# Performance work log

Measured on AMD Instinct MI355X. Metric: run time of the kernel, lower is better.

The kernel has to match this reference:

```python
import jax, jax.numpy as jnp
import numpy as np

WS = 7        # window size (square)
SH = 3        # shift size
NH = 8        # num heads
N = WS * WS   # tokens per window


def _rel_pos_index():
    coords = np.stack(np.meshgrid(np.arange(WS), np.arange(WS), indexing='ij'))
    cf = coords.reshape(2, -1)                      # (2, N)
    rel = cf[:, :, None] - cf[:, None, :]           # (2, N, N)
    rel = rel.transpose(1, 2, 0)
    rel[:, :, 0] += WS - 1
    rel[:, :, 1] += WS - 1
    rel[:, :, 0] *= 2 * WS - 1
    return rel.sum(-1)                              # (N, N) int


def _attn_mask(pH, pW):
    img = np.zeros((pH, pW), dtype=np.float32)
    h_sl = [(0, pH - WS), (pH - WS, pH - SH), (pH - SH, pH)]
    w_sl = [(0, pW - WS), (pW - WS, pW - SH), (pW - SH, pW)]
    cnt = 0
    for h0, h1 in h_sl:
        for w0, w1 in w_sl:
            img[h0:h1, w0:w1] = cnt
            cnt += 1
    m = img.reshape(pH // WS, WS, pW // WS, WS).transpose(0, 2, 1, 3).reshape(-1, N)
    diff = m[:, None, :] - m[:, :, None]            # (nw, N, N)
    return np.where(diff != 0, -100.0, 0.0).astype(np.float32)


def setup_inputs() -> dict:
    key = jax.random.key(0)
    ks = jax.random.split(key, 6)
    C = 256
    return {
        'x': jax.random.normal(ks[0], (32, 56, 56, C), dtype=jnp.float32),
        'qkv_weight': jax.random.normal(ks[1], (3 * C, C), dtype=jnp.float32) * 0.02,
        'qkv_bias': jax.random.normal(ks[2], (3 * C,), dtype=jnp.float32) * 0.02,
        'proj_weight': jax.random.normal(ks[3], (C, C), dtype=jnp.float32) * 0.02,
        'proj_bias': jax.random.normal(ks[4], (C,), dtype=jnp.float32) * 0.02,
        'rpb_table': jax.random.normal(ks[5], ((2 * WS - 1) ** 2, NH), dtype=jnp.float32) * 0.02,
    }


def reference(x, qkv_weight, qkv_bias, proj_weight, proj_bias, rpb_table):
    B, H, W, C = x.shape
    hd = C // NH
    pad_r = (WS - W % WS) % WS
    pad_b = (WS - H % WS) % WS
    xp = jnp.pad(x, ((0, 0), (0, pad_b), (0, pad_r), (0, 0)))
    pH, pW = H + pad_b, W + pad_r
    xp = jnp.roll(xp, shift=(-SH, -SH), axis=(1, 2))
    nw = (pH // WS) * (pW // WS)
    # window partition -> (B*nw, N, C)
    xw = xp.reshape(B, pH // WS, WS, pW // WS, WS, C)
    xw = xw.transpose(0, 1, 3, 2, 4, 5).reshape(B * nw, N, C)
    # qkv projection
    qkv = xw @ qkv_weight.T + qkv_bias                      # (B*nw, N, 3C)
    qkv = qkv.reshape(B * nw, N, 3, NH, hd).transpose(2, 0, 3, 1, 4)
    q, k, v = qkv[0], qkv[1], qkv[2]                        # (B*nw, NH, N, hd)
    q = q * (hd ** -0.5)
    attn = jnp.einsum('bhnd,bhmd->bhnm', q, k)              # (B*nw, NH, N, N)
    # relative position bias
    idx = jnp.asarray(_rel_pos_index())
    bias = rpb_table[idx].transpose(2, 0, 1)                # (NH, N, N)
    attn = attn + bias[None]
    # shift mask
    mask = jnp.asarray(_attn_mask(pH, pW))                  # (nw, N, N)
    attn = attn.reshape(B, nw, NH, N, N) + mask[None, :, None]
    attn = jax.nn.softmax(attn.reshape(B * nw, NH, N, N), axis=-1)
    out = jnp.einsum('bhnm,bhmd->bhnd', attn, v)            # (B*nw, NH, N, hd)
    out = out.transpose(0, 2, 1, 3).reshape(B * nw, N, C)
    out = out @ proj_weight.T + proj_bias
    # window reverse
    out = out.reshape(B, pH // WS, pW // WS, WS, WS, C)
    out = out.transpose(0, 1, 3, 2, 4, 5).reshape(B, pH, pW, C)
    out = jnp.roll(out, shift=(SH, SH), axis=(1, 2))
    return out[:, :H, :W, :]
```

## Files before the change

kernel.cpp:

```cpp
#include <hip/hip_runtime.h>
#include <hip/hip_bf16.h>

typedef __attribute__((ext_vector_type(4))) float f32x4;
typedef __attribute__((ext_vector_type(8))) short s16x8;
typedef __attribute__((ext_vector_type(4))) short s16x4;
typedef __attribute__((ext_vector_type(4))) unsigned uintx4;

#define LBS 264
#define VTS 72
#define LOS 132

__device__ __forceinline__ unsigned cvt2bf(float a, float b) {
    unsigned r;
    asm("v_cvt_pk_bf16_f32 %0, %1, %2" : "=v"(r) : "v"(a), "v"(b));
    return r;
}

__device__ __forceinline__ s16x4 pk4bf(float a, float b, float c, float d) {
    uint2 t = { cvt2bf(a, b), cvt2bf(c, d) };
    return __builtin_bit_cast(s16x4, t);
}

__device__ __forceinline__ s16x8 expand_z(s16x4 c) {
    uint2 u = __builtin_bit_cast(uint2, c);
    uintx4 r = { u.x & 0xFFFFu, u.x >> 16, u.y & 0xFFFFu, u.y >> 16 };
    return __builtin_bit_cast(s16x8, r);
}

__global__ void prep_kernel(const float* __restrict__ qw, const float* __restrict__ pw,
                            const float* __restrict__ rpb,
                            short* __restrict__ wqkv, short* __restrict__ wproj,
                            float* __restrict__ bm) {
    int idx = blockIdx.x * blockDim.x + threadIdx.x;
    if (idx < 65536) {
        const float* src = (idx < 49152) ? (qw + idx * 4) : (pw + (idx - 49152) * 4);
        unsigned* dst = (unsigned*)((idx < 49152) ? (wqkv + idx * 4) : (wproj + (idx - 49152) * 4));
        const f32x4 v = *(const f32x4*)src;
        uint2 o = { cvt2bf(v.x, v.y), cvt2bf(v.z, v.w) };
        *(uint2*)dst = o;
    } else {
        int k = idx - 65536;
        int j = k & 63;
        int i = (k >> 6) & 63;
        int h = (k >> 12) & 7;
        int c = k >> 15;
        int cy = c >> 1, cx = c & 1;
        float v;
        if (j >= 49) {
            v = -1e9f;
        } else {
            int ic = i > 48 ? 48 : i;
            int yi = ic / 7, xi = ic % 7;
            int yj = j / 7, xj = j % 7;
            float bias = rpb[((yi - yj + 6) * 13 + (xi - xj + 6)) * 8 + h];
            int ri = (cy ? (yi < 4 ? 1 : 2) : 0) * 3 + (cx ? (xi < 4 ? 1 : 2) : 0);
            int rj = (cy ? (yj < 4 ? 1 : 2) : 0) * 3 + (cx ? (xj < 4 ? 1 : 2) : 0);
            float mask = (ri != rj) ? -100.0f : 0.0f;
            v = (bias + mask) * 1.4426950408889634f;
        }
        bm[k] = v;
    }
}

__global__ __launch_bounds__(512, 2)
void attn_kernel(const float* __restrict__ x,
                 const float* __restrict__ qkv_bias,
                 const short* __restrict__ wqkv,
                 const float* __restrict__ bm,
                 unsigned short* __restrict__ la) {
    __shared__ __align__(16) short buf[64 * LBS];
    __shared__ __align__(16) short lvt[128 * VTS];
    __shared__ float lml[8 * 64];

    const int tid  = threadIdx.x;
    const int w    = tid >> 6;
    const int lane = tid & 63;
    const int il   = lane & 15;
    const int gl   = lane >> 4;
    const int hl   = w >> 1;
    const int jh   = w & 1;

    const int hg  = blockIdx.x & 1;
    const int win = blockIdx.x >> 1;
    const int wid = win & 63;
    const int b   = win >> 6;
    const int wy  = wid >> 3, wx = wid & 7;

    for (int i = tid; i < 4096; i += 512) {
        int t = i >> 6, c4 = (i & 63) << 2;
        uint2 o;
        if (t < 49) {
            int ty = t / 7, tx = t % 7;
            int R = wy * 7 + ty + 3; if (R >= 56) R -= 56;
            int C = wx * 7 + tx + 3; if (C >= 56) C -= 56;
            const f32x4 v = *(const f32x4*)(x + (((b * 56 + R) * 56 + C) << 8) + c4);
            o.x = cvt2bf(v.x, v.y); o.y = cvt2bf(v.z, v.w);
        } else {
            o.x = 0; o.y = 0;
        }
        *(uint2*)&buf[t * LBS + c4] = o;
    }
    __syncthreads();

    {
        f32x4 acc[4][3];
        #pragma unroll
        for (int mi = 0; mi < 4; mi++)
            #pragma unroll
            for (int t = 0; t < 3; t++) acc[mi][t] = (f32x4){0.f, 0.f, 0.f, 0.f};
        __builtin_amdgcn_s_setprio(1);
        for (int k0 = 0; k0 < 256; k0 += 32) {
            s16x8 a[4];
            #pragma unroll
            for (int mi = 0; mi < 4; mi++)
                a[mi] = *(const s16x8*)&buf[(mi * 16 + il) * LBS + k0 + 8 * gl];
            #pragma unroll
            for (int t = 0; t < 3; t++) {
                s16x8 bfr = *(const s16x8*)(wqkv + (t * 256 + hg * 128 + 16 * w + il) * 256 + k0 + 8 * gl);
                #pragma unroll
                for (int mi = 0; mi < 4; mi++)
                    acc[mi][t] = __builtin_amdgcn_mfma_f32_16x16x32_bf16(a[mi], bfr, acc[mi][t], 0, 0, 0);
            }
        }
        __builtin_amdgcn_s_setprio(0);
        {
            float bv = qkv_bias[512 + hg * 128 + 16 * w + il];
            #pragma unroll
            for (int mi = 0; mi < 4; mi++)
                *(s16x4*)&lvt[(16 * w + il) * VTS + mi * 16 + gl * 4] =
                    pk4bf(acc[mi][2][0] + bv, acc[mi][2][1] + bv,
                          acc[mi][2][2] + bv, acc[mi][2][3] + bv);
        }
        __syncthreads();
        {
            const float QSCL = 0.17677669529663687f * 1.4426950408889634f;
            float bq_ = qkv_bias[hg * 128 + 16 * w + il];
            float bk_ = qkv_bias[256 + hg * 128 + 16 * w + il];
            #pragma unroll
            for (int mi = 0; mi < 4; mi++)
                #pragma unroll
                for (int r = 0; r < 4; r++) {
                    int row = mi * 16 + gl * 4 + r;
                    unsigned u = cvt2bf((acc[mi][0][r] + bq_) * QSCL, acc[mi][1][r] + bk_);
                    buf[row * LBS + 16 * w + il] = (short)u;
                    buf[row * LBS + 128 + 16 * w + il] = (short)(u >> 16);
                }
        }
    }
    __syncthreads();

    const int cls = ((wy == 7) ? 2 : 0) + ((wx == 7) ? 1 : 0);
    const float* bmp = bm + ((cls * 8 + hg * 4 + hl) * 64) * 64;

    f32x4 s[2][4];
    #pragma unroll
    for (int mi = 0; mi < 2; mi++)
        #pragma unroll
        for (int ni = 0; ni < 4; ni++)
            s[mi][ni] = *(const f32x4*)&bmp[(ni * 16 + il) * 64 + jh * 32 + mi * 16 + gl * 4];
    {
        s16x8 bq[4];
        #pragma unroll
        for (int ni = 0; ni < 4; ni++)
            bq[ni] = *(const s16x8*)&buf[(ni * 16 + il) * LBS + hl * 32 + 8 * gl];
        __builtin_amdgcn_s_setprio(1);
        #pragma unroll
        for (int mi = 0; mi < 2; mi++) {
            s16x8 ak = *(const s16x8*)&buf[(jh * 32 + mi * 16 + il) * LBS + 128 + hl * 32 + 8 * gl];
            #pragma unroll
            for (int ni = 0; ni < 4; ni++)
                s[mi][ni] = __builtin_amdgcn_mfma_f32_16x16x32_bf16(ak, bq[ni], s[mi][ni], 0, 0, 0);
        }
        __builtin_amdgcn_s_setprio(0);
    }
    float l[4] = { 0.f, 0.f, 0.f, 0.f };
    s16x4 pkd[2][4];
    #pragma unroll
    for (int mi = 0; mi < 2; mi++)
        #pragma unroll
        for (int ni = 0; ni < 4; ni++) {
            float p0 = exp2f(s[mi][ni][0]);
            float p1 = exp2f(s[mi][ni][1]);
            float p2 = exp2f(s[mi][ni][2]);
            float p3 = exp2f(s[mi][ni][3]);
            l[ni] += (p0 + p1) + (p2 + p3);
            pkd[mi][ni] = pk4bf(p0, p1, p2, p3);
        }
    #pragma unroll
    for (int ni = 0; ni < 4; ni++) {
        l[ni] += __shfl_xor(l[ni], 16);
        l[ni] += __shfl_xor(l[ni], 32);
    }
    if (jh == 0 && gl == 0) {
        #pragma unroll
        for (int ni = 0; ni < 4; ni++) lml[(hl * 2) * 64 + ni * 16 + il] = l[ni];
    }
    __syncthreads();

    f32x4 o[2][4];
    #pragma unroll
    for (int md = 0; md < 2; md++)
        #pragma unroll
        for (int ni = 0; ni < 4; ni++) o[md][ni] = (f32x4){0.f, 0.f, 0.f, 0.f};
    __builtin_amdgcn_s_setprio(1);
    #pragma unroll
    for (int mi = 0; mi < 2; mi++) {
        s16x8 av[2];
        #pragma unroll
        for (int md = 0; md < 2; md++)
            av[md] = expand_z(*(const s16x4*)&lvt[(hl * 32 + md * 16 + il) * VTS + jh * 32 + mi * 16 + 4 * gl]);
        #pragma unroll
        for (int ni = 0; ni < 4; ni++) {
            s16x8 bp = expand_z(pkd[mi][ni]);
            #pragma unroll
            for (int md = 0; md < 2; md++)
                o[md][ni] = __builtin_amdgcn_mfma_f32_16x16x32_bf16(av[md], bp, o[md][ni], 0, 0, 0);
        }
    }
    __builtin_amdgcn_s_setprio(0);
    float* lout = (float*)buf;
    if (jh == 0) {
        #pragma unroll
        for (int md = 0; md < 2; md++)
            #pragma unroll
            for (int ni = 0; ni < 4; ni++)
                *(f32x4*)&lout[(ni * 16 + il) * LOS + hl * 32 + md * 16 + gl * 4] = o[md][ni];
    }
    __syncthreads();
    if (jh == 1) {
        float sc[4];
        #pragma unroll
        for (int ni = 0; ni < 4; ni++)
            sc[ni] = __builtin_amdgcn_rcpf(l[ni] + lml[(hl * 2) * 64 + ni * 16 + il]);
        #pragma unroll
        for (int ni = 0; ni < 4; ni++) {
            int i = ni * 16 + il;
            if (i < 49) {
                #pragma unroll
                for (int md = 0; md < 2; md++) {
                    f32x4 t = *(const f32x4*)&lout[i * LOS + hl * 32 + md * 16 + gl * 4];
                    uint2 pk = { cvt2bf((t.x + o[md][ni][0]) * sc[ni], (t.y + o[md][ni][1]) * sc[ni]),
                                 cvt2bf((t.z + o[md][ni][2]) * sc[ni], (t.w + o[md][ni][3]) * sc[ni]) };
                    *(uint2*)&la[(win * 49 + i) * 256 + hg * 128 + hl * 32 + md * 16 + gl * 4] = pk;
                }
            }
        }
    }
}

__global__ __launch_bounds__(512, 2)
void proj_kernel(const unsigned short* __restrict__ la,
                 const float* __restrict__ proj_bias,
                 const short* __restrict__ wproj,
                 float* __restrict__ out) {
    __shared__ __align__(16) short buf[64 * LBS];

    const int tid  = threadIdx.x;
    const int w    = tid >> 6;
    const int lane = tid & 63;
    const int il   = lane & 15;
    const int gl   = lane >> 4;

    const int win = blockIdx.x;
    const int wid = win & 63;
    const int b   = win >> 6;
    const int wy  = wid >> 3, wx = wid & 7;

    for (int i = tid; i < 2048; i += 512) {
        int t = i >> 5, c8 = (i & 31) << 3;
        uintx4 v = (t < 49) ? *(const uintx4*)&la[(win * 49 + t) * 256 + c8]
                            : (uintx4){0u, 0u, 0u, 0u};
        *(uintx4*)&buf[t * LBS + c8] = v;
    }
    __syncthreads();

    f32x4 acc[4][2];
    #pragma unroll
    for (int mi = 0; mi < 4; mi++)
        #pragma unroll
        for (int ni = 0; ni < 2; ni++) acc[mi][ni] = (f32x4){0.f, 0.f, 0.f, 0.f};
    __builtin_amdgcn_s_setprio(1);
    for (int k0 = 0; k0 < 256; k0 += 32) {
        s16x8 a[4];
        #pragma unroll
        for (int mi = 0; mi < 4; mi++)
            a[mi] = *(const s16x8*)&buf[(mi * 16 + il) * LBS + k0 + 8 * gl];
        #pragma unroll
        for (int ni = 0; ni < 2; ni++) {
            s16x8 bw = *(const s16x8*)(wproj + (32 * w + 16 * ni + il) * 256 + k0 + 8 * gl);
            #pragma unroll
            for (int mi = 0; mi < 4; mi++)
                acc[mi][ni] = __builtin_amdgcn_mfma_f32_16x16x32_bf16(a[mi], bw, acc[mi][ni], 0, 0, 0);
        }
    }
    __builtin_amdgcn_s_setprio(0);
    __syncthreads();
    #pragma unroll
    for (int ni = 0; ni < 2; ni++) {
        int oc = 32 * w + 16 * ni + il;
        float pb = proj_bias[oc];
        #pragma unroll
        for (int mi = 0; mi < 4; mi++)
            #pragma unroll
            for (int r = 0; r < 4; r++) {
                int t = mi * 16 + gl * 4 + r;
                if (t < 49) {
                    unsigned u = cvt2bf(acc[mi][ni][r] + pb, 0.f);
                    buf[t * LBS + oc] = (short)u;
                }
            }
    }
    __syncthreads();
    for (int i = tid; i < 1568; i += 512) {
        int t = i >> 5, c8 = (i & 31) << 3;
        uintx4 u = *(const uintx4*)&buf[t * LBS + c8];
        f32x4 v0, v1;
        v0.x = __builtin_bit_cast(float, u.x << 16);
        v0.y = __builtin_bit_cast(float, u.x & 0xFFFF0000u);
        v0.z = __builtin_bit_cast(float, u.y << 16);
        v0.w = __builtin_bit_cast(float, u.y & 0xFFFF0000u);
        v1.x = __builtin_bit_cast(float, u.z << 16);
        v1.y = __builtin_bit_cast(float, u.z & 0xFFFF0000u);
        v1.z = __builtin_bit_cast(float, u.w << 16);
        v1.w = __builtin_bit_cast(float, u.w & 0xFFFF0000u);
        int ty = t / 7, tx = t % 7;
        int R = wy * 7 + ty + 3; if (R >= 56) R -= 56;
        int C = wx * 7 + tx + 3; if (C >= 56) C -= 56;
        float* op = out + (((b * 56 + R) * 56 + C) << 8) + c8;
        *(f32x4*)op = v0;
        *(f32x4*)(op + 4) = v1;
    }
}

extern "C" void kernel_launch(void* const* d_in, const int* in_sizes, int n_in,
                              void* d_out, int out_size, void* d_ws, size_t ws_size,
                              hipStream_t stream) {
    const float* x   = (const float*)d_in[0];
    const float* qw  = (const float*)d_in[1];
    const float* qb  = (const float*)d_in[2];
    const float* pw  = (const float*)d_in[3];
    const float* pb  = (const float*)d_in[4];
    const float* rpb = (const float*)d_in[5];

    short* wqkv  = (short*)d_ws;
    short* wproj = wqkv + 768 * 256;
    float* bmt   = (float*)((char*)d_ws + 524288);
    unsigned short* lat = (unsigned short*)((char*)d_ws + 2097152);

    prep_kernel<<<768, 256, 0, stream>>>(qw, pw, rpb, wqkv, wproj, bmt);
    attn_kernel<<<4096, 512, 0, stream>>>(x, qb, wqkv, bmt, lat);
    proj_kernel<<<2048, 512, 0, stream>>>(lat, pb, wproj, (float*)d_out);
}
```

Measured before the change: 234.8 us.

## Split QKV projection into a row-contiguous kernel writing windowed bf16 Q/K/V

Moves the QKV GEMM out of the attention kernel into a new kernel that processes one contiguous image row (56 tokens) per block, so the fp32 input is read with coalesced row accesses instead of shifted window gathers. It then scatters bf16 Q/K and V into per-window, per-head-group buffers that the attention kernel loads and transposes into LDS, and the attention output reuses the Q/K buffer. Also drops the s_setprio hints. This adds an extra kernel launch and a bf16 round trip of Q/K/V through global memory.

```diff
diff --git a/kernel.cpp b/kernel.cpp
--- a/kernel.cpp
+++ b/kernel.cpp
@@ -7,6 +7,7 @@
 typedef __attribute__((ext_vector_type(4))) unsigned uintx4;
 
 #define LBS 264
+#define VBS 136
 #define VTS 72
 #define LOS 132
 
@@ -63,42 +64,42 @@
 }
 
 __global__ __launch_bounds__(512, 2)
-void attn_kernel(const float* __restrict__ x,
-                 const float* __restrict__ qkv_bias,
-                 const short* __restrict__ wqkv,
-                 const float* __restrict__ bm,
-                 unsigned short* __restrict__ la) {
+void qkv_kernel(const float* __restrict__ x,
+                const float* __restrict__ qkv_bias,
+                const short* __restrict__ wqkv,
+                unsigned short* __restrict__ qkg,
+                unsigned short* __restrict__ vg) {
     __shared__ __align__(16) short buf[64 * LBS];
-    __shared__ __align__(16) short lvt[128 * VTS];
-    __shared__ float lml[8 * 64];
+    __shared__ __align__(16) short vbufL[64 * VBS];
 
     const int tid  = threadIdx.x;
     const int w    = tid >> 6;
     const int lane = tid & 63;
     const int il   = lane & 15;
     const int gl   = lane >> 4;
-    const int hl   = w >> 1;
-    const int jh   = w & 1;
-
-    const int hg  = blockIdx.x & 1;
-    const int win = blockIdx.x >> 1;
-    const int wid = win & 63;
-    const int b   = win >> 6;
-    const int wy  = wid >> 3, wx = wid & 7;
-
-    for (int i = tid; i < 4096; i += 512) {
-        int t = i >> 6, c4 = (i & 63) << 2;
-        uint2 o;
-        if (t < 49) {
-            int ty = t / 7, tx = t % 7;
-            int R = wy * 7 + ty + 3; if (R >= 56) R -= 56;
-            int C = wx * 7 + tx + 3; if (C >= 56) C -= 56;
-            const f32x4 v = *(const f32x4*)(x + (((b * 56 + R) * 56 + C) << 8) + c4);
-            o.x = cvt2bf(v.x, v.y); o.y = cvt2bf(v.z, v.w);
-        } else {
-            o.x = 0; o.y = 0;
-        }
-        *(uint2*)&buf[t * LBS + c4] = o;
+
+    const int hg     = blockIdx.x & 1;
+    const int rowIdx = blockIdx.x >> 1;
+    const int R      = rowIdx % 56;
+    int rr = R + 53; if (rr >= 56) rr -= 56;
+    const int wy = rr / 7, ty = rr % 7;
+    const int winRowBase = ((rowIdx / 56) << 6) + (wy << 3);
+    const int posRowBase = ty * 7;
+
+    {
+        const int t0 = tid >> 3;
+        const int cb = (tid & 7) << 2;
+        const float* xrow = x + (size_t)(rowIdx * 56 + (t0 < 56 ? t0 : 0)) * 256;
+        #pragma unroll
+        for (int j = 0; j < 8; j++) {
+            int c4 = cb + 32 * j;
+            uint2 o = { 0u, 0u };
+            if (t0 < 56) {
+                const f32x4 v = *(const f32x4*)(xrow + c4);
+                o.x = cvt2bf(v.x, v.y); o.y = cvt2bf(v.z, v.w);
+            }
+            *(uint2*)&buf[t0 * LBS + c4] = o;
+        }
     }
     __syncthreads();
 
@@ -108,7 +109,6 @@
         for (int mi = 0; mi < 4; mi++)
             #pragma unroll
             for (int t = 0; t < 3; t++) acc[mi][t] = (f32x4){0.f, 0.f, 0.f, 0.f};
-        __builtin_amdgcn_s_setprio(1);
         for (int k0 = 0; k0 < 256; k0 += 32) {
             s16x8 a[4];
             #pragma unroll
@@ -122,14 +122,15 @@
                     acc[mi][t] = __builtin_amdgcn_mfma_f32_16x16x32_bf16(a[mi], bfr, acc[mi][t], 0, 0, 0);
             }
         }
-        __builtin_amdgcn_s_setprio(0);
         {
             float bv = qkv_bias[512 + hg * 128 + 16 * w + il];
             #pragma unroll
             for (int mi = 0; mi < 4; mi++)
-                *(s16x4*)&lvt[(16 * w + il) * VTS + mi * 16 + gl * 4] =
-                    pk4bf(acc[mi][2][0] + bv, acc[mi][2][1] + bv,
-                          acc[mi][2][2] + bv, acc[mi][2][3] + bv);
+                #pragma unroll
+                for (int r = 0; r < 4; r++) {
+                    unsigned u = cvt2bf(acc[mi][2][r] + bv, 0.f);
+                    vbufL[(mi * 16 + gl * 4 + r) * VBS + 16 * w + il] = (short)u;
+                }
         }
         __syncthreads();
         {
@@ -149,6 +150,63 @@
     }
     __syncthreads();
 
+    for (int i = tid; i < 1792; i += 512) {
+        int t = i >> 5, ch = (i & 31) << 3;
+        int cc = t + 53; if (cc >= 56) cc -= 56;
+        int wx = cc / 7, tx = cc % 7;
+        int dstrow = ((winRowBase + wx) * 2 + hg) * 49 + posRowBase + tx;
+        *(uintx4*)&qkg[(size_t)dstrow * 256 + ch] = *(const uintx4*)&buf[t * LBS + ch];
+    }
+    for (int i = tid; i < 896; i += 512) {
+        int t = i >> 4, ch = (i & 15) << 3;
+        int cc = t + 53; if (cc >= 56) cc -= 56;
+        int wx = cc / 7, tx = cc % 7;
+        int dstrow = ((winRowBase + wx) * 2 + hg) * 49 + posRowBase + tx;
+        *(uintx4*)&vg[(size_t)dstrow * 128 + ch] = *(const uintx4*)&vbufL[t * VBS + ch];
+    }
+}
+
+__global__ __launch_bounds__(512, 2)
+void attn_kernel(const float* __restrict__ bm,
+                 unsigned short* __restrict__ qkg,
+                 const unsigned short* __restrict__ vg) {
+    __shared__ __align__(16) short buf[64 * LBS];
+    __shared__ __align__(16) short lvt[128 * VTS];
+    __shared__ float lml[8 * 64];
+
+    const int tid  = threadIdx.x;
+    const int w    = tid >> 6;
+    const int lane = tid & 63;
+    const int il   = lane & 15;
+    const int gl   = lane >> 4;
+    const int hl   = w >> 1;
+    const int jh   = w & 1;
+
+    const int hg  = blockIdx.x & 1;
+    const int win = blockIdx.x >> 1;
+    const int wid = win & 63;
+    const int wy  = wid >> 3, wx = wid & 7;
+    const long whg = win * 2 + hg;
+
+    for (int i = tid; i < 2048; i += 512) {
+        int t = i >> 5, ch = (i & 31) << 3;
+        uintx4 v = (t < 49) ? *(const uintx4*)&qkg[(whg * 49 + t) * 256 + ch]
+                            : (uintx4){0u, 0u, 0u, 0u};
+        *(uintx4*)&buf[t * LBS + ch] = v;
+    }
+    for (int i = tid; i < 1024; i += 512) {
+        int t = i >> 4, ch = (i & 15) << 3;
+        uintx4 v = (t < 49) ? *(const uintx4*)&vg[(whg * 49 + t) * 128 + ch]
+                            : (uintx4){0u, 0u, 0u, 0u};
+        unsigned uu[4] = { v.x, v.y, v.z, v.w };
+        #pragma unroll
+        for (int e = 0; e < 4; e++) {
+            lvt[(ch + 2 * e) * VTS + t]     = (short)(uu[e] & 0xFFFFu);
+            lvt[(ch + 2 * e + 1) * VTS + t] = (short)(uu[e] >> 16);
+        }
+    }
+    __syncthreads();
+
     const int cls = ((wy == 7) ? 2 : 0) + ((wx == 7) ? 1 : 0);
     const float* bmp = bm + ((cls * 8 + hg * 4 + hl) * 64) * 64;
 
@@ -163,7 +221,6 @@
         #pragma unroll
         for (int ni = 0; ni < 4; ni++)
             bq[ni] = *(const s16x8*)&buf[(ni * 16 + il) * LBS + hl * 32 + 8 * gl];
-        __builtin_amdgcn_s_setprio(1);
         #pragma unroll
         for (int mi = 0; mi < 2; mi++) {
             s16x8 ak = *(const s16x8*)&buf[(jh * 32 + mi * 16 + il) * LBS + 128 + hl * 32 + 8 * gl];
@@ -171,7 +228,6 @@
             for (int ni = 0; ni < 4; ni++)
                 s[mi][ni] = __builtin_amdgcn_mfma_f32_16x16x32_bf16(ak, bq[ni], s[mi][ni], 0, 0, 0);
         }
-        __builtin_amdgcn_s_setprio(0);
     }
     float l[4] = { 0.f, 0.f, 0.f, 0.f };
     s16x4 pkd[2][4];
@@ -202,7 +258,6 @@
     for (int md = 0; md < 2; md++)
         #pragma unroll
         for (int ni = 0; ni < 4; ni++) o[md][ni] = (f32x4){0.f, 0.f, 0.f, 0.f};
-    __builtin_amdgcn_s_setprio(1);
     #pragma unroll
     for (int mi = 0; mi < 2; mi++) {
         s16x8 av[2];
@@ -217,7 +272,6 @@
                 o[md][ni] = __builtin_amdgcn_mfma_f32_16x16x32_bf16(av[md], bp, o[md][ni], 0, 0, 0);
         }
     }
-    __builtin_amdgcn_s_setprio(0);
     float* lout = (float*)buf;
     if (jh == 0) {
         #pragma unroll
@@ -241,7 +295,7 @@
                     f32x4 t = *(const f32x4*)&lout[i * LOS + hl * 32 + md * 16 + gl * 4];
                     uint2 pk = { cvt2bf((t.x + o[md][ni][0]) * sc[ni], (t.y + o[md][ni][1]) * sc[ni]),
                                  cvt2bf((t.z + o[md][ni][2]) * sc[ni], (t.w + o[md][ni][3]) * sc[ni]) };
-                    *(uint2*)&la[(win * 49 + i) * 256 + hg * 128 + hl * 32 + md * 16 + gl * 4] = pk;
+                    *(uint2*)&qkg[(whg * 49 + i) * 256 + hl * 32 + md * 16 + gl * 4] = pk;
                 }
             }
         }
@@ -249,7 +303,7 @@
 }
 
 __global__ __launch_bounds__(512, 2)
-void proj_kernel(const unsigned short* __restrict__ la,
+void proj_kernel(const unsigned short* __restrict__ qkg,
                  const float* __restrict__ proj_bias,
                  const short* __restrict__ wproj,
                  float* __restrict__ out) {
@@ -267,10 +321,17 @@
     const int wy  = wid >> 3, wx = wid & 7;
 
     for (int i = tid; i < 2048; i += 512) {
-        int t = i >> 5, c8 = (i & 31) << 3;
-        uintx4 v = (t < 49) ? *(const uintx4*)&la[(win * 49 + t) * 256 + c8]
-                            : (uintx4){0u, 0u, 0u, 0u};
-        *(uintx4*)&buf[t * LBS + c8] = v;
+        int t = i >> 5;
+        int chunk = i & 31;
+        int ch = chunk << 3;
+        uintx4 v = { 0u, 0u, 0u, 0u };
+        if (t < 49) {
+            if (chunk < 16)
+                v = *(const uintx4*)&qkg[((size_t)(win * 2) * 49 + t) * 256 + ch];
+            else
+                v = *(const uintx4*)&qkg[((size_t)(win * 2 + 1) * 49 + t) * 256 + (ch - 128)];
+        }
+        *(uintx4*)&buf[t * LBS + ch] = v;
     }
     __syncthreads();
 
@@ -279,7 +340,6 @@
     for (int mi = 0; mi < 4; mi++)
         #pragma unroll
         for (int ni = 0; ni < 2; ni++) acc[mi][ni] = (f32x4){0.f, 0.f, 0.f, 0.f};
-    __builtin_amdgcn_s_setprio(1);
     for (int k0 = 0; k0 < 256; k0 += 32) {
         s16x8 a[4];
         #pragma unroll
@@ -293,7 +353,6 @@
                 acc[mi][ni] = __builtin_amdgcn_mfma_f32_16x16x32_bf16(a[mi], bw, acc[mi][ni], 0, 0, 0);
         }
     }
-    __builtin_amdgcn_s_setprio(0);
     __syncthreads();
     #pragma unroll
     for (int ni = 0; ni < 2; ni++) {
@@ -345,9 +404,11 @@
     short* wqkv  = (short*)d_ws;
     short* wproj = wqkv + 768 * 256;
     float* bmt   = (float*)((char*)d_ws + 524288);
-    unsigned short* lat = (unsigned short*)((char*)d_ws + 2097152);
+    unsigned short* qkg = (unsigned short*)((char*)d_ws + 2097152);
+    unsigned short* vg  = (unsigned short*)((char*)d_ws + 104857600);
 
     prep_kernel<<<768, 256, 0, stream>>>(qw, pw, rpb, wqkv, wproj, bmt);
-    attn_kernel<<<4096, 512, 0, stream>>>(x, qb, wqkv, bmt, lat);
-    proj_kernel<<<2048, 512, 0, stream>>>(lat, pb, wproj, (float*)d_out);
-}
+    qkv_kernel<<<3584, 512, 0, stream>>>(x, qb, wqkv, qkg, vg);
+    attn_kernel<<<4096, 512, 0, stream>>>(bmt, qkg, vg);
+    proj_kernel<<<2048, 512, 0, stream>>>(qkg, pb, wproj, (float*)d_out);
+}
```

After: 334.3 us. +42.4%, slower.
